# Kernel tuning notes

Measured on AMD Instinct MI355X. Metric: run time of the kernel, lower is better.

Reference implementation:

```python
import jax, jax.numpy as jnp
import numpy as np

B, T, C = 1, 4096, 1024
H = 16
D = C // H  # head_dim = 64


def setup_inputs() -> dict:
    key = jax.random.key(0)
    ks = jax.random.split(key, 9)
    s = 1.0 / np.sqrt(C)
    return {
        "x": jax.random.normal(ks[0], (B, T, C), dtype=jnp.float32),
        "Wq": jax.random.normal(ks[1], (C, C), dtype=jnp.float32) * s,
        "bq": jnp.zeros((C,), dtype=jnp.float32),
        "Wk": jax.random.normal(ks[2], (C, C), dtype=jnp.float32) * s,
        "bk": jnp.zeros((C,), dtype=jnp.float32),
        "Wv": jax.random.normal(ks[3], (C, C), dtype=jnp.float32) * s,
        "bv": jnp.zeros((C,), dtype=jnp.float32),
        "Wo": jax.random.normal(ks[4], (C, C), dtype=jnp.float32) * s,
        "bo": jnp.zeros((C,), dtype=jnp.float32),
    }


def reference(x, Wq, bq, Wk, bk, Wv, bv, Wo, bo):
    # QKV projections (torch Linear: y = x @ W.T + b)
    q = x @ Wq.T + bq
    k = x @ Wk.T + bk
    v = x @ Wv.T + bv
    # [B,T,C] -> [B,H,T,D]
    q = q.reshape(B, T, H, D).transpose(0, 2, 1, 3)
    k = k.reshape(B, T, H, D).transpose(0, 2, 1, 3)
    v = v.reshape(B, T, H, D).transpose(0, 2, 1, 3)
    scale = 1.0 / jnp.sqrt(jnp.asarray(D, dtype=q.dtype))
    scores = jnp.einsum("bhqd,bhkd->bhqk", q, k) * scale  # [B,H,T,T]
    attn = jax.nn.softmax(scores, axis=-1)
    out = jnp.einsum("bhqk,bhkd->bhqd", attn, v)  # [B,H,T,D]
    out = out.transpose(0, 2, 1, 3).reshape(B, T, C)
    return out @ Wo.T + bo
```

## Files before the change

### kernel.cpp

```cpp
#include <hip/hip_runtime.h>
#include <stdint.h>

#define T_SEQ 4096
#define CDIM  1024
#define NH    16
#define DH    64

typedef _Float16 half8 __attribute__((ext_vector_type(8)));
typedef _Float16 half4 __attribute__((ext_vector_type(4)));
typedef float    f32x4 __attribute__((ext_vector_type(4)));

#if __has_builtin(__builtin_amdgcn_exp2f)
#define EXP2F(x) __builtin_amdgcn_exp2f(x)
#else
#define EXP2F(x) exp2f(x)
#endif

#define MFMA_K32(a, b, c) __builtin_amdgcn_mfma_f32_16x16x32_f16(a, b, c, 0, 0, 0)
#define MFMA_K16(a, b, c) __builtin_amdgcn_mfma_f32_16x16x16f16(a, b, c, 0, 0, 0)

__device__ __forceinline__ void gl_lds16(const void* g, void* l) {
  __builtin_amdgcn_global_load_lds(
      (const __attribute__((address_space(1))) uint32_t*)g,
      (__attribute__((address_space(3))) uint32_t*)l, 16, 0, 0);
}

__global__ void cvt_all_kernel(const float* __restrict__ w0, const float* __restrict__ w1,
                               const float* __restrict__ w2, const float* __restrict__ w3,
                               const float* __restrict__ x,
                               _Float16* __restrict__ o0, _Float16* __restrict__ o1,
                               _Float16* __restrict__ o2, _Float16* __restrict__ o3,
                               _Float16* __restrict__ xo) {
  int y = blockIdx.y;
  const float* src;
  _Float16* dst;
  if (y < 4) {
    src = (y == 0) ? w0 : (y == 1) ? w1 : (y == 2) ? w2 : w3;
    dst = (y == 0) ? o0 : (y == 1) ? o1 : (y == 2) ? o2 : o3;
  } else {
    src = x  + (size_t)(y - 4) * (CDIM * CDIM);
    dst = xo + (size_t)(y - 4) * (CDIM * CDIM);
  }
  int i = (blockIdx.x * blockDim.x + threadIdx.x) * 8;
  float4 f0 = *(const float4*)(src + i);
  float4 f1 = *(const float4*)(src + i + 4);
  half8 h = { (_Float16)f0.x, (_Float16)f0.y, (_Float16)f0.z, (_Float16)f0.w,
              (_Float16)f1.x, (_Float16)f1.y, (_Float16)f1.z, (_Float16)f1.w };
  *(half8*)(dst + i) = h;
}

__device__ __forceinline__ void gemm_core(const _Float16* __restrict__ A,
                                          const _Float16* __restrict__ Bm,
                                          _Float16* As, _Float16* Bs,
                                          int bm, int bn,
                                          f32x4 (&acc)[4][4]) {
  const int tid  = threadIdx.x;
  const int lane = tid & 63;
  const int wave = tid >> 6;
  const int waveM = wave >> 1, waveN = wave & 1;
  const int quad = lane >> 4, c16 = lane & 15;

  const int rs0 = wave * 32 + (lane >> 2);
  const int rs1 = rs0 + 16;
  const int dm0 = ((lane & 3) ^ ((rs0 >> 1) & 3)) * 8;
  const int dm1 = ((lane & 3) ^ ((rs1 >> 1) & 3)) * 8;

  const _Float16* gA0 = A  + (size_t)(bm * 128 + rs0) * CDIM + dm0;
  const _Float16* gA1 = A  + (size_t)(bm * 128 + rs1) * CDIM + dm1;
  const _Float16* gB0 = Bm + (size_t)(bn * 128 + rs0) * CDIM + dm0;
  const _Float16* gB1 = Bm + (size_t)(bn * 128 + rs1) * CDIM + dm1;
  _Float16* lA0 = As + wave * 1024;
  _Float16* lA1 = lA0 + 512;
  _Float16* lB0 = Bs + wave * 1024;
  _Float16* lB1 = lB0 + 512;

  const int xsw  = (c16 >> 1) & 3;
  const int offA = (waveM * 64 + c16) * 32 + ((quad ^ xsw) * 8);
  const int offB = (waveN * 64 + c16) * 32 + ((quad ^ xsw) * 8);

  for (int kk = 0; kk < 32; ++kk) {
    gl_lds16(gA0, lA0);
    gl_lds16(gA1, lA1);
    gl_lds16(gB0, lB0);
    gl_lds16(gB1, lB1);
    __syncthreads();
    half8 a[4], b[4];
#pragma unroll
    for (int i = 0; i < 4; ++i) a[i] = *(const half8*)(As + offA + i * 512);
#pragma unroll
    for (int i = 0; i < 4; ++i) b[i] = *(const half8*)(Bs + offB + i * 512);
#pragma unroll
    for (int mi = 0; mi < 4; ++mi)
#pragma unroll
      for (int ni = 0; ni < 4; ++ni)
        acc[mi][ni] = MFMA_K32(a[mi], b[ni], acc[mi][ni]);
    gA0 += 32; gA1 += 32; gB0 += 32; gB1 += 32;
    __syncthreads();
  }
}

__device__ __forceinline__ void gemm_core64(const _Float16* __restrict__ A,
                                            const _Float16* __restrict__ Bm,
                                            _Float16* As, _Float16* Bs,
                                            int bm, int bn,
                                            f32x4 (&acc)[2][4]) {
  const int tid  = threadIdx.x;
  const int lane = tid & 63;
  const int wave = tid >> 6;
  const int waveM = wave >> 1, waveN = wave & 1;
  const int quad = lane >> 4, c16 = lane & 15;

  const int rsA = wave * 16 + (lane >> 2);
  const int dmA = ((lane & 3) ^ ((rsA >> 1) & 3)) * 8;
  const int rs0 = wave * 32 + (lane >> 2);
  const int rs1 = rs0 + 16;
  const int dm0 = ((lane & 3) ^ ((rs0 >> 1) & 3)) * 8;
  const int dm1 = ((lane & 3) ^ ((rs1 >> 1) & 3)) * 8;

  const _Float16* gA0 = A  + (size_t)(bm * 64  + rsA) * CDIM + dmA;
  const _Float16* gB0 = Bm + (size_t)(bn * 128 + rs0) * CDIM + dm0;
  const _Float16* gB1 = Bm + (size_t)(bn * 128 + rs1) * CDIM + dm1;
  _Float16* lA0 = As + wave * 512;
  _Float16* lB0 = Bs + wave * 1024;
  _Float16* lB1 = lB0 + 512;

  const int xsw  = (c16 >> 1) & 3;
  const int offA = (waveM * 32 + c16) * 32 + ((quad ^ xsw) * 8);
  const int offB = (waveN * 64 + c16) * 32 + ((quad ^ xsw) * 8);

  for (int kk = 0; kk < 32; ++kk) {
    gl_lds16(gA0, lA0);
    gl_lds16(gB0, lB0);
    gl_lds16(gB1, lB1);
    __syncthreads();
    half8 a[2], b[4];
#pragma unroll
    for (int i = 0; i < 2; ++i) a[i] = *(const half8*)(As + offA + i * 512);
#pragma unroll
    for (int i = 0; i < 4; ++i) b[i] = *(const half8*)(Bs + offB + i * 512);
#pragma unroll
    for (int mi = 0; mi < 2; ++mi)
#pragma unroll
      for (int ni = 0; ni < 4; ++ni)
        acc[mi][ni] = MFMA_K32(a[mi], b[ni], acc[mi][ni]);
    gA0 += 32; gB0 += 32; gB1 += 32;
    __syncthreads();
  }
}

__global__ __launch_bounds__(256) void qkv_gemm(
    const _Float16* __restrict__ xh,
    const _Float16* __restrict__ wqh, const _Float16* __restrict__ wkh, const _Float16* __restrict__ wvh,
    const float* __restrict__ bq, const float* __restrict__ bk, const float* __restrict__ bv,
    _Float16* __restrict__ qh, _Float16* __restrict__ kh, _Float16* __restrict__ vfs) {
  __shared__ __align__(16) _Float16 As[128 * 32];
  __shared__ __align__(16) _Float16 Bs[128 * 32];
  const int z = blockIdx.z;
  const _Float16* W   = (z == 0) ? wqh : ((z == 1) ? wkh : wvh);
  const float*    bias = (z == 0) ? bq  : ((z == 1) ? bk  : bv);

  f32x4 acc[4][4];
  const f32x4 zf = {0.f, 0.f, 0.f, 0.f};
#pragma unroll
  for (int i = 0; i < 4; ++i)
#pragma unroll
    for (int j = 0; j < 4; ++j) acc[i][j] = zf;

  gemm_core(xh, W, As, Bs, blockIdx.x, blockIdx.y, acc);

  const int lane = threadIdx.x & 63, wave = threadIdx.x >> 6;
  const int waveM = wave >> 1, waveN = wave & 1;
  const int quad = lane >> 4, c16 = lane & 15;
  const int rowb = blockIdx.x * 128 + waveM * 64;
  const int colb = blockIdx.y * 128 + waveN * 64;

  float bsv[4];
#pragma unroll
  for (int ni = 0; ni < 4; ++ni) bsv[ni] = bias[colb + ni * 16 + c16];

  if (z < 2) {
    _Float16* outp = (z == 0) ? qh : kh;
    const float scl = (z == 0) ? 0.18033688011112042f : 1.0f;
#pragma unroll
    for (int mi = 0; mi < 4; ++mi)
#pragma unroll
      for (int ni = 0; ni < 4; ++ni) {
        int col = colb + ni * 16 + c16;
        int hh = col >> 6, dd = col & 63;
#pragma unroll
        for (int r = 0; r < 4; ++r) {
          int row = rowb + mi * 16 + quad * 4 + r;
          outp[(size_t)(hh * T_SEQ + row) * DH + dd] = (_Float16)((acc[mi][ni][r] + bsv[ni]) * scl);
        }
      }
  } else {
    const int kt = rowb >> 6;
#pragma unroll
    for (int mi = 0; mi < 4; ++mi)
#pragma unroll
      for (int ni = 0; ni < 4; ++ni) {
        int col = colb + ni * 16 + c16;
        int hh = col >> 6, dd = col & 63;
        int db = dd >> 4, cv = dd & 15;
        half4 h4;
#pragma unroll
        for (int r = 0; r < 4; ++r) h4[r] = (_Float16)(acc[mi][ni][r] + bsv[ni]);
        *(half4*)(vfs + (size_t)hh * (T_SEQ * 64) + (size_t)kt * 4096
                      + (mi * 4 + db) * 256 + quad * 64 + cv * 4) = h4;
      }
  }
}

__global__ __launch_bounds__(256) void out_gemm(
    const _Float16* __restrict__ ctx, const _Float16* __restrict__ woh,
    const float* __restrict__ bo, float* __restrict__ out) {
  __shared__ __align__(16) _Float16 As[64 * 32];
  __shared__ __align__(16) _Float16 Bs[128 * 32];
  f32x4 acc[2][4];
  const f32x4 zf = {0.f, 0.f, 0.f, 0.f};
#pragma unroll
  for (int i = 0; i < 2; ++i)
#pragma unroll
    for (int j = 0; j < 4; ++j) acc[i][j] = zf;

  gemm_core64(ctx, woh, As, Bs, blockIdx.x, blockIdx.y, acc);

  const int lane = threadIdx.x & 63, wave = threadIdx.x >> 6;
  const int waveM = wave >> 1, waveN = wave & 1;
  const int quad = lane >> 4, c16 = lane & 15;
  const int rowb = blockIdx.x * 64 + waveM * 32;
  const int colb = blockIdx.y * 128 + waveN * 64;

  float bsv[4];
#pragma unroll
  for (int ni = 0; ni < 4; ++ni) bsv[ni] = bo[colb + ni * 16 + c16];

#pragma unroll
  for (int mi = 0; mi < 2; ++mi)
#pragma unroll
    for (int ni = 0; ni < 4; ++ni) {
      int col = colb + ni * 16 + c16;
#pragma unroll
      for (int r = 0; r < 4; ++r) {
        int row = rowb + mi * 16 + quad * 4 + r;
        out[(size_t)row * CDIM + col] = acc[mi][ni][r] + bsv[ni];
      }
    }
}

__global__ __launch_bounds__(256) void attn_kernel(
    const _Float16* __restrict__ qh, const _Float16* __restrict__ kh,
    const _Float16* __restrict__ vfs, _Float16* __restrict__ ctx) {
  __shared__ __align__(16) _Float16 Ks[2][64 * 64];

  const int tid = threadIdx.x, lane = tid & 63, wave = tid >> 6;
  const int quad = lane >> 4, c16 = lane & 15;
  const int h = blockIdx.y;
  const int qw = blockIdx.x * 128 + wave * 32;

  half8 qf[2][2];
#pragma unroll
  for (int qg = 0; qg < 2; ++qg)
#pragma unroll
    for (int c = 0; c < 2; ++c)
      qf[qg][c] = *(const half8*)(qh + (size_t)(h * T_SEQ + qw + qg * 16 + c16) * DH + c * 32 + quad * 8);

  const int rs0 = wave * 16 + (lane >> 3);
  const int rs1 = rs0 + 8;
  const int dm0 = ((lane & 7) ^ (rs0 & 7)) * 8;
  const int dm1 = ((lane & 7) ^ (rs1 & 7)) * 8;
  const _Float16* gK0 = kh + (size_t)(h * T_SEQ + rs0) * DH + dm0;
  const _Float16* gK1 = kh + (size_t)(h * T_SEQ + rs1) * DH + dm1;
  const int lo0 = wave * 1024, lo1 = wave * 1024 + 512;

  const _Float16* vb = vfs + (size_t)h * (T_SEQ * 64) + lane * 4;

  f32x4 o[2][4];
  f32x4 lacc[2];
  const f32x4 zf = {0.f, 0.f, 0.f, 0.f};
#pragma unroll
  for (int qg = 0; qg < 2; ++qg) {
#pragma unroll
    for (int db = 0; db < 4; ++db) o[qg][db] = zf;
    lacc[qg] = zf;
  }
  const half4 ones4 = { (_Float16)1, (_Float16)1, (_Float16)1, (_Float16)1 };

  gl_lds16(gK0, &Ks[0][lo0]);
  gl_lds16(gK1, &Ks[0][lo1]);
  gK0 += 64 * DH; gK1 += 64 * DH;
  __syncthreads();

  for (int kt = 0; kt < 64; ++kt) {
    const int b = kt & 1;

    half4 av[16];
    {
      const _Float16* vp = vb + (size_t)kt * 4096;
#pragma unroll
      for (int f = 0; f < 16; ++f) av[f] = *(const half4*)(vp + f * 256);
    }

    if (kt < 63) {
      gl_lds16(gK0, &Ks[b ^ 1][lo0]);
      gl_lds16(gK1, &Ks[b ^ 1][lo1]);
      gK0 += 64 * DH; gK1 += 64 * DH;
    }
    const _Float16* Kb = &Ks[b][0];

    const f32x4 minit = {-16.f, -16.f, -16.f, -16.f};
    f32x4 s[2][4];
#pragma unroll
    for (int qg = 0; qg < 2; ++qg)
#pragma unroll
      for (int kb = 0; kb < 4; ++kb) s[qg][kb] = minit;
#pragma unroll
    for (int c = 0; c < 2; ++c) {
#pragma unroll
      for (int kb = 0; kb < 4; ++kb) {
        int key = kb * 16 + c16;
        half8 ak = *(const half8*)(Kb + key * 64 + (((c * 4 + quad) ^ (key & 7)) * 8));
        s[0][kb] = MFMA_K32(ak, qf[0][c], s[0][kb]);
        s[1][kb] = MFMA_K32(ak, qf[1][c], s[1][kb]);
      }
    }

    half4 p[2][4];
#pragma unroll
    for (int qg = 0; qg < 2; ++qg)
#pragma unroll
      for (int kb = 0; kb < 4; ++kb)
#pragma unroll
        for (int r = 0; r < 4; ++r) p[qg][kb][r] = (_Float16)EXP2F(s[qg][kb][r]);

#pragma unroll
    for (int kb = 0; kb < 4; ++kb) {
      lacc[0] = MFMA_K16(ones4, p[0][kb], lacc[0]);
      lacc[1] = MFMA_K16(ones4, p[1][kb], lacc[1]);
    }

#pragma unroll
    for (int kb = 0; kb < 4; ++kb)
#pragma unroll
      for (int db = 0; db < 4; ++db) {
        o[0][db] = MFMA_K16(av[kb * 4 + db], p[0][kb], o[0][db]);
        o[1][db] = MFMA_K16(av[kb * 4 + db], p[1][kb], o[1][db]);
      }

    __syncthreads();
  }

  _Float16* Pw = ((_Float16*)Ks) + wave * (32 * 64);
#pragma unroll
  for (int qg = 0; qg < 2; ++qg) {
    float inv = 1.f / lacc[qg][0];
#pragma unroll
    for (int db = 0; db < 4; ++db) {
      half4 h4;
#pragma unroll
      for (int r = 0; r < 4; ++r) h4[r] = (_Float16)(o[qg][db][r] * inv);
      int row = qg * 16 + c16;
      int g   = db * 2 + (quad >> 1);
      *(half4*)(Pw + row * 64 + ((g ^ (row & 7)) * 8) + (quad & 1) * 4) = h4;
    }
  }
  __syncthreads();
  const int q = lane >> 1, hv = lane & 1;
#pragma unroll
  for (int i = 0; i < 4; ++i) {
    int g = hv * 4 + i;
    half8 vv = *(const half8*)(Pw + q * 64 + ((g ^ (q & 7)) * 8));
    *(half8*)(ctx + (size_t)(qw + q) * CDIM + h * DH + g * 8) = vv;
  }
}

extern "C" void kernel_launch(void* const* d_in, const int* in_sizes, int n_in,
                              void* d_out, int out_size, void* d_ws, size_t ws_size,
                              hipStream_t stream) {
  const float* x  = (const float*)d_in[0];
  const float* Wq = (const float*)d_in[1];
  const float* bq = (const float*)d_in[2];
  const float* Wk = (const float*)d_in[3];
  const float* bk = (const float*)d_in[4];
  const float* Wv = (const float*)d_in[5];
  const float* bv = (const float*)d_in[6];
  const float* Wo = (const float*)d_in[7];
  const float* bo = (const float*)d_in[8];
  float* out = (float*)d_out;

  char* ws = (char*)d_ws;
  _Float16* xh  = (_Float16*)(ws);
  _Float16* qh  = (_Float16*)(ws + ((size_t)8  << 20));
  _Float16* kh  = (_Float16*)(ws + ((size_t)16 << 20));
  _Float16* vfs = (_Float16*)(ws + ((size_t)24 << 20));
  _Float16* wqh = (_Float16*)(ws + ((size_t)32 << 20));
  _Float16* wkh = (_Float16*)(ws + ((size_t)34 << 20));
  _Float16* wvh = (_Float16*)(ws + ((size_t)36 << 20));
  _Float16* woh = (_Float16*)(ws + ((size_t)38 << 20));
  _Float16* ctx = xh;

  cvt_all_kernel<<<dim3(512, 8), 256, 0, stream>>>(Wq, Wk, Wv, Wo, x,
                                                   wqh, wkh, wvh, woh, xh);
  qkv_gemm<<<dim3(32, 8, 3), 256, 0, stream>>>(xh, wqh, wkh, wvh, bq, bk, bv, qh, kh, vfs);
  attn_kernel<<<dim3(32, 16), 256, 0, stream>>>(qh, kh, vfs, ctx);
  out_gemm<<<dim3(64, 8), 256, 0, stream>>>(ctx, woh, bo, out);
}
```

Baseline: 257.1 us.

## Stage transposed V through LDS and use K32 MFMA for PV via LDS-staged P

The QKV GEMM now writes V transposed per head (d-major over T), and the attention kernel double-buffers V tiles into LDS with async global-to-LDS loads alongside K. It no longer reads V fragments directly from global memory each step. The softmax probabilities are written to a per-wave swizzled LDS buffer and read back as 8-wide fragments, so PV and the row-sum use 16x16x32 MFMAs instead of 16x16x16 ones. The loop is unrolled by two with explicit buffer indices, and launch bounds request two blocks per CU. In exchange, LDS use grows (K, V and P buffers), which may cap occupancy, and there is an extra LDS round-trip for P.

```diff
diff --git a/kernel.cpp b/kernel.cpp
--- a/kernel.cpp
+++ b/kernel.cpp
@@ -17,7 +17,6 @@
 #endif
 
 #define MFMA_K32(a, b, c) __builtin_amdgcn_mfma_f32_16x16x32_f16(a, b, c, 0, 0, 0)
-#define MFMA_K16(a, b, c) __builtin_amdgcn_mfma_f32_16x16x16f16(a, b, c, 0, 0, 0)
 
 __device__ __forceinline__ void gl_lds16(const void* g, void* l) {
   __builtin_amdgcn_global_load_lds(
@@ -152,7 +151,7 @@
     const _Float16* __restrict__ xh,
     const _Float16* __restrict__ wqh, const _Float16* __restrict__ wkh, const _Float16* __restrict__ wvh,
     const float* __restrict__ bq, const float* __restrict__ bk, const float* __restrict__ bv,
-    _Float16* __restrict__ qh, _Float16* __restrict__ kh, _Float16* __restrict__ vfs) {
+    _Float16* __restrict__ qh, _Float16* __restrict__ kh, _Float16* __restrict__ vth) {
   __shared__ __align__(16) _Float16 As[128 * 32];
   __shared__ __align__(16) _Float16 Bs[128 * 32];
   const int z = blockIdx.z;
@@ -194,19 +193,16 @@
         }
       }
   } else {
-    const int kt = rowb >> 6;
 #pragma unroll
     for (int mi = 0; mi < 4; ++mi)
 #pragma unroll
       for (int ni = 0; ni < 4; ++ni) {
-        int col = colb + ni * 16 + c16;
-        int hh = col >> 6, dd = col & 63;
-        int db = dd >> 4, cv = dd & 15;
+        int col  = colb + ni * 16 + c16;
+        int row0 = rowb + mi * 16 + quad * 4;
         half4 h4;
 #pragma unroll
         for (int r = 0; r < 4; ++r) h4[r] = (_Float16)(acc[mi][ni][r] + bsv[ni]);
-        *(half4*)(vfs + (size_t)hh * (T_SEQ * 64) + (size_t)kt * 4096
-                      + (mi * 4 + db) * 256 + quad * 64 + cv * 4) = h4;
+        *(half4*)(vth + (size_t)col * T_SEQ + row0) = h4;
       }
   }
 }
@@ -248,10 +244,12 @@
     }
 }
 
-__global__ __launch_bounds__(256) void attn_kernel(
+__global__ __launch_bounds__(256, 2) void attn_kernel(
     const _Float16* __restrict__ qh, const _Float16* __restrict__ kh,
-    const _Float16* __restrict__ vfs, _Float16* __restrict__ ctx) {
+    const _Float16* __restrict__ vth, _Float16* __restrict__ ctx) {
   __shared__ __align__(16) _Float16 Ks[2][64 * 64];
+  __shared__ __align__(16) _Float16 Vs[2][64 * 64];
+  __shared__ __align__(16) _Float16 Ps[4][32 * 64];
 
   const int tid = threadIdx.x, lane = tid & 63, wave = tid >> 6;
   const int quad = lane >> 4, c16 = lane & 15;
@@ -269,11 +267,13 @@
   const int rs1 = rs0 + 8;
   const int dm0 = ((lane & 7) ^ (rs0 & 7)) * 8;
   const int dm1 = ((lane & 7) ^ (rs1 & 7)) * 8;
-  const _Float16* gK0 = kh + (size_t)(h * T_SEQ + rs0) * DH + dm0;
-  const _Float16* gK1 = kh + (size_t)(h * T_SEQ + rs1) * DH + dm1;
+  const _Float16* gK0 = kh  + (size_t)(h * T_SEQ + rs0) * DH + dm0;
+  const _Float16* gK1 = kh  + (size_t)(h * T_SEQ + rs1) * DH + dm1;
+  const _Float16* gV0 = vth + (size_t)(h * DH + rs0) * T_SEQ + dm0;
+  const _Float16* gV1 = vth + (size_t)(h * DH + rs1) * T_SEQ + dm1;
   const int lo0 = wave * 1024, lo1 = wave * 1024 + 512;
 
-  const _Float16* vb = vfs + (size_t)h * (T_SEQ * 64) + lane * 4;
+  _Float16* Pw = &Ps[wave][0];
 
   f32x4 o[2][4];
   f32x4 lacc[2];
@@ -284,29 +284,26 @@
     for (int db = 0; db < 4; ++db) o[qg][db] = zf;
     lacc[qg] = zf;
   }
-  const half4 ones4 = { (_Float16)1, (_Float16)1, (_Float16)1, (_Float16)1 };
+  const half8 ones8 = { (_Float16)1, (_Float16)1, (_Float16)1, (_Float16)1,
+                        (_Float16)1, (_Float16)1, (_Float16)1, (_Float16)1 };
 
   gl_lds16(gK0, &Ks[0][lo0]);
   gl_lds16(gK1, &Ks[0][lo1]);
-  gK0 += 64 * DH; gK1 += 64 * DH;
+  gl_lds16(gV0, &Vs[0][lo0]);
+  gl_lds16(gV1, &Vs[0][lo1]);
+  gK0 += 64 * DH; gK1 += 64 * DH; gV0 += 64; gV1 += 64;
   __syncthreads();
 
-  for (int kt = 0; kt < 64; ++kt) {
-    const int b = kt & 1;
-
-    half4 av[16];
-    {
-      const _Float16* vp = vb + (size_t)kt * 4096;
-#pragma unroll
-      for (int f = 0; f < 16; ++f) av[f] = *(const half4*)(vp + f * 256);
-    }
-
-    if (kt < 63) {
-      gl_lds16(gK0, &Ks[b ^ 1][lo0]);
-      gl_lds16(gK1, &Ks[b ^ 1][lo1]);
-      gK0 += 64 * DH; gK1 += 64 * DH;
-    }
-    const _Float16* Kb = &Ks[b][0];
+  auto step = [&](int bc, int bn, bool pf) {
+    if (pf) {
+      gl_lds16(gK0, &Ks[bn][lo0]);
+      gl_lds16(gK1, &Ks[bn][lo1]);
+      gl_lds16(gV0, &Vs[bn][lo0]);
+      gl_lds16(gV1, &Vs[bn][lo1]);
+      gK0 += 64 * DH; gK1 += 64 * DH; gV0 += 64; gV1 += 64;
+    }
+    const _Float16* Kb = &Ks[bc][0];
+    const _Float16* Vb = &Vs[bc][0];
 
     const f32x4 minit = {-16.f, -16.f, -16.f, -16.f};
     f32x4 s[2][4];
@@ -325,32 +322,49 @@
       }
     }
 
-    half4 p[2][4];
-#pragma unroll
-    for (int qg = 0; qg < 2; ++qg)
-#pragma unroll
-      for (int kb = 0; kb < 4; ++kb)
-#pragma unroll
-        for (int r = 0; r < 4; ++r) p[qg][kb][r] = (_Float16)EXP2F(s[qg][kb][r]);
-
-#pragma unroll
-    for (int kb = 0; kb < 4; ++kb) {
-      lacc[0] = MFMA_K16(ones4, p[0][kb], lacc[0]);
-      lacc[1] = MFMA_K16(ones4, p[1][kb], lacc[1]);
-    }
-
-#pragma unroll
-    for (int kb = 0; kb < 4; ++kb)
+#pragma unroll
+    for (int qg = 0; qg < 2; ++qg) {
+#pragma unroll
+      for (int kb = 0; kb < 4; ++kb) {
+        half4 pk;
+#pragma unroll
+        for (int r = 0; r < 4; ++r) pk[r] = (_Float16)EXP2F(s[qg][kb][r]);
+        int row = qg * 16 + c16;
+        int g   = kb * 2 + (quad >> 1);
+        *(half4*)(Pw + row * 64 + ((g ^ (row & 7)) * 8) + (quad & 1) * 4) = pk;
+      }
+    }
+
+    half8 av[2][4];
+#pragma unroll
+    for (int kb32 = 0; kb32 < 2; ++kb32)
 #pragma unroll
       for (int db = 0; db < 4; ++db) {
-        o[0][db] = MFMA_K16(av[kb * 4 + db], p[0][kb], o[0][db]);
-        o[1][db] = MFMA_K16(av[kb * 4 + db], p[1][kb], o[1][db]);
-      }
-
-    __syncthreads();
-  }
-
-  _Float16* Pw = ((_Float16*)Ks) + wave * (32 * 64);
+        int d = db * 16 + c16;
+        av[kb32][db] = *(const half8*)(Vb + d * 64 + (((kb32 * 4 + quad) ^ (d & 7)) * 8));
+      }
+
+#pragma unroll
+    for (int qg = 0; qg < 2; ++qg) {
+      int row = qg * 16 + c16;
+#pragma unroll
+      for (int kb32 = 0; kb32 < 2; ++kb32) {
+        half8 bp = *(const half8*)(Pw + row * 64 + (((kb32 * 4 + quad) ^ (row & 7)) * 8));
+        lacc[qg] = MFMA_K32(ones8, bp, lacc[qg]);
+#pragma unroll
+        for (int db = 0; db < 4; ++db)
+          o[qg][db] = MFMA_K32(av[kb32][db], bp, o[qg][db]);
+      }
+    }
+  };
+
+  for (int it = 0; it < 32; ++it) {
+    step(0, 1, true);
+    __syncthreads();
+    step(1, 0, it < 31);
+    __syncthreads();
+  }
+
 #pragma unroll
   for (int qg = 0; qg < 2; ++qg) {
     float inv = 1.f / lacc[qg][0];
@@ -364,7 +378,6 @@
       *(half4*)(Pw + row * 64 + ((g ^ (row & 7)) * 8) + (quad & 1) * 4) = h4;
     }
   }
-  __syncthreads();
   const int q = lane >> 1, hv = lane & 1;
 #pragma unroll
   for (int i = 0; i < 4; ++i) {
@@ -392,7 +405,7 @@
   _Float16* xh  = (_Float16*)(ws);
   _Float16* qh  = (_Float16*)(ws + ((size_t)8  << 20));
   _Float16* kh  = (_Float16*)(ws + ((size_t)16 << 20));
-  _Float16* vfs = (_Float16*)(ws + ((size_t)24 << 20));
+  _Float16* vth = (_Float16*)(ws + ((size_t)24 << 20));
   _Float16* wqh = (_Float16*)(ws + ((size_t)32 << 20));
   _Float16* wkh = (_Float16*)(ws + ((size_t)34 << 20));
   _Float16* wvh = (_Float16*)(ws + ((size_t)36 << 20));
@@ -401,7 +414,7 @@
 
   cvt_all_kernel<<<dim3(512, 8), 256, 0, stream>>>(Wq, Wk, Wv, Wo, x,
                                                    wqh, wkh, wvh, woh, xh);
-  qkv_gemm<<<dim3(32, 8, 3), 256, 0, stream>>>(xh, wqh, wkh, wvh, bq, bk, bv, qh, kh, vfs);
-  attn_kernel<<<dim3(32, 16), 256, 0, stream>>>(qh, kh, vfs, ctx);
+  qkv_gemm<<<dim3(32, 8, 3), 256, 0, stream>>>(xh, wqh, wkh, wvh, bq, bk, bv, qh, kh, vth);
+  attn_kernel<<<dim3(32, 16), 256, 0, stream>>>(qh, kh, vth, ctx);
   out_gemm<<<dim3(64, 8), 256, 0, stream>>>(ctx, woh, bo, out);
 }
```

After: 223.9 us. 1.15x faster.
